# Performance work log

Hardware: AMD Instinct MI355X
Metric: run time of the kernel (lower is better)

## Reference

```python
import jax, jax.numpy as jnp
import numpy as np
import math

B, N, D, H = 4, 512, 256, 8
DH = D // H


def setup_inputs() -> dict:
    key = jax.random.key(0)
    ks = jax.random.split(key, 10)
    s = 1.0 / math.sqrt(D)
    return {
        "h": jax.random.normal(ks[0], (B, N, D), jnp.float32),
        "p": jax.random.uniform(ks[1], (B, N, 2), jnp.float32) * 100.0,
        "side_id": jax.random.randint(ks[2], (B, N), 0, 2),
        "mask": jnp.ones((B, N), dtype=bool),
        # weights stored in 'apply' orientation: y = x @ W (+ b)
        "Wq": jax.random.normal(ks[3], (D, D), jnp.float32) * s,
        "Wk": jax.random.normal(ks[4], (D, D), jnp.float32) * s,
        "Wv": jax.random.normal(ks[5], (D, D), jnp.float32) * s,
        "Wo": jax.random.normal(ks[6], (D, D), jnp.float32) * s,
        "W1": jax.random.normal(ks[7], (4, D), jnp.float32) * 0.5,
        "b1": jnp.zeros((D,), jnp.float32),
        "W2": jax.random.normal(ks[8], (D, H), jnp.float32) * s,
        "b2": jnp.zeros((H,), jnp.float32),
    }


def reference(h, p, side_id, mask, Wq, Wk, Wv, Wo, W1, b1, W2, b2):
    # zero out masked players
    h = jnp.where(mask[..., None], h, 0.0)  # [B,N,D]

    q = (h @ Wq).reshape(B, N, H, DH)
    k = (h @ Wk).reshape(B, N, H, DH)
    v = (h @ Wv).reshape(B, N, H, DH)

    # pairwise relative-position features [B,N,N,4]
    dp = p[:, :, None, :] - p[:, None, :, :]               # [B,N,N,2]
    dist = jnp.clip(jnp.linalg.norm(dp, axis=-1, keepdims=True), 1e-6)
    is_team = (side_id[:, :, None] == side_id[:, None, :]).astype(h.dtype)[..., None]
    feat = jnp.concatenate([dp, dist, is_team], axis=-1)

    # 2-layer bias MLP -> per-head bias [B,H,N,N]
    hid = jax.nn.relu(feat @ W1 + b1)                      # [B,N,N,D]
    bias = (hid @ W2 + b2).transpose(0, 3, 1, 2)           # [B,H,N,N]

    logits = jnp.einsum('bihd,bjhd->bhij', q, k) / math.sqrt(DH)
    logits = logits + bias
    logits = logits + jnp.where(mask, 0.0, -1e9)[:, None, None, :]  # key mask

    attn = jax.nn.softmax(logits, axis=-1)                 # dropout = identity (eval)
    out = jnp.einsum('bhij,bjhd->bihd', attn, v).reshape(B, N, D)
    return out @ Wo
```

## Files before the change

### kernel.cpp

```cpp
#include <hip/hip_runtime.h>
#include <math.h>

#define BB 4
#define NN 512
#define DD 256
#define HH 8
#define BND (BB*NN*DD)

typedef _Float16 h2 __attribute__((ext_vector_type(2)));
typedef _Float16 f16x4 __attribute__((ext_vector_type(4)));
typedef float    f32x4 __attribute__((ext_vector_type(4)));

static __device__ __forceinline__ h2 u2h(unsigned u) { return __builtin_bit_cast(h2, u); }
static __device__ __forceinline__ h2 pk2(float a, float b) {
    h2 r; r[0] = (_Float16)a; r[1] = (_Float16)b; return r;
}
static __device__ __forceinline__ unsigned pk2u(float a, float b) {
    return __builtin_bit_cast(unsigned, pk2(a, b));
}
static __device__ __forceinline__ h2 pkz(float a, float b) {
    return __builtin_bit_cast(h2, __builtin_amdgcn_cvt_pkrtz(a, b));
}
static __device__ __forceinline__ float dot2(h2 a, h2 b, float c) {
    return __builtin_amdgcn_fdot2(a, b, c, false);
}

__global__ __launch_bounds__(256) void pack_wt(
    const float* __restrict__ Wq, const float* __restrict__ Wk,
    const float* __restrict__ Wv, const float* __restrict__ Wo,
    _Float16* __restrict__ wt)
{
    __shared__ float T[64][65];
    const int t  = threadIdx.x;
    const int nb = blockIdx.x >> 2;
    const int kb = blockIdx.x & 3;
    const int tn = t & 63;
    const int tr = t >> 6;
    const int nbase = nb * 64;
    const float* W = (nbase < 256) ? Wq : (nbase < 512) ? Wk : (nbase < 768) ? Wv : Wo;
    const int noff = nbase & 255;
    #pragma unroll
    for (int r = 0; r < 16; ++r) {
        const int kl = tr*16 + r;
        T[kl][tn] = W[(size_t)(kb*64 + kl)*DD + noff + tn];
    }
    __syncthreads();
    #pragma unroll
    for (int r = 0; r < 16; ++r) {
        const int nl = tr*16 + r;
        wt[(size_t)(nbase + nl)*DD + kb*64 + tn] = (_Float16)T[tn][nl];
    }
}

__global__ __launch_bounds__(64) void gemm_qkv(
    const float* __restrict__ hg, const int* __restrict__ mask,
    const _Float16* __restrict__ wt,
    _Float16* __restrict__ q16, _Float16* __restrict__ k16, _Float16* __restrict__ v16h)
{
    const int l  = threadIdx.x;
    const int lo = l & 15, g = l >> 4;
    const int bid = blockIdx.x;
    const int rt = bid / 24, ct = bid % 24;
    const int R0 = rt*16, C0 = ct*32;
    const int row = R0 + lo;
    const float msc = (mask[row] != 0) ? 1.f : 0.f;

    const float*    xrow = hg + (size_t)row*DD;
    const _Float16* w0   = wt + (size_t)(C0 + lo)*DD;
    const _Float16* w1   = wt + (size_t)(C0 + 16 + lo)*DD;
    f32x4 ac0 = {0.f,0.f,0.f,0.f}, ac1 = {0.f,0.f,0.f,0.f};
    #pragma unroll
    for (int kk = 0; kk < 16; ++kk) {
        const float4 xv = *(const float4*)(xrow + kk*16 + g*4);
        f16x4 a;
        a[0] = (_Float16)(xv.x * msc);
        a[1] = (_Float16)(xv.y * msc);
        a[2] = (_Float16)(xv.z * msc);
        a[3] = (_Float16)(xv.w * msc);
        const f16x4 b0 = *(const f16x4*)(w0 + kk*16 + g*4);
        const f16x4 b1 = *(const f16x4*)(w1 + kk*16 + g*4);
        ac0 = __builtin_amdgcn_mfma_f32_16x16x16f16(a, b0, ac0, 0, 0, 0);
        ac1 = __builtin_amdgcn_mfma_f32_16x16x16f16(a, b1, ac1, 0, 0, 0);
    }
    const float qscale = 0.17677669529663687f;
    #pragma unroll
    for (int ci = 0; ci < 2; ++ci) {
        const f32x4 ac = ci ? ac1 : ac0;
        const int col = C0 + ci*16 + lo;
        const int seg = col >> 8;
        const int cc  = col & 255;
        #pragma unroll
        for (int r = 0; r < 4; ++r) {
            const int ro = R0 + g*4 + r;
            const float val = ac[r];
            if (seg == 0)      q16[(size_t)ro*DD + cc] = (_Float16)val;
            else if (seg == 1) k16[(size_t)ro*DD + cc] = (_Float16)(val * qscale);
            else               v16h[((size_t)(ro >> 1)*DD + cc)*2 + (ro & 1)] = (_Float16)val;
        }
    }
}

__global__ __launch_bounds__(256, 3) void bias_qk(
    const _Float16* __restrict__ q16, const _Float16* __restrict__ k16,
    const float* __restrict__ p, const int* __restrict__ side, const int* __restrict__ mask,
    const float* __restrict__ W1, const float* __restrict__ b1,
    const float* __restrict__ W2, const float* __restrict__ b2,
    unsigned* __restrict__ logitsH)
{
    __shared__ float bsm[4][16*132];
    __shared__ float pis[16][2];
    __shared__ int   sis[16];

    const int t  = threadIdx.x;
    const int w  = t >> 6;
    const int l  = t & 63;
    const int lo = l & 15;
    const int g  = l >> 4;

    const int bid = blockIdx.x;
    const int b   = bid >> 8;
    const int it  = (bid >> 3) & 31;
    const int je  = bid & 7;
    const int i0  = it * 16;
    const int jb  = je * 64 + w * 16;
    const int j   = jb + lo;

    if (t < 16) {
        const float2 pp = ((const float2*)p)[b*NN + i0 + t];
        pis[t][0] = pp.x; pis[t][1] = pp.y;
        sis[t] = side[b*NN + i0 + t];
    }
    __syncthreads();

    const f16x4 z4 = {(_Float16)0.f,(_Float16)0.f,(_Float16)0.f,(_Float16)0.f};
    const f32x4 zf = {0.f,0.f,0.f,0.f};
    const h2 zz = {(_Float16)0.f, (_Float16)0.f};

    f16x4 a1[16];
    #pragma unroll
    for (int m = 0; m < 16; ++m) {
        const int hid = m*16 + lo;
        f16x4 v = z4;
        const float w0 = W1[hid], w1 = W1[256+hid], w2 = W1[512+hid], w3 = W1[768+hid];
        const float bb1 = b1[hid];
        if (g == 0) { v[0]=(_Float16)w0; v[1]=(_Float16)w1; v[2]=(_Float16)w2; v[3]=(_Float16)w3; }
        else if (g == 1) { v[0]=(_Float16)bb1; }
        a1[m] = v;
    }
    f16x4 a2[16];
    #pragma unroll
    for (int s = 0; s < 16; ++s) {
        const int kb4 = s*16 + g*4;
        const int hs  = lo & 7;
        f16x4 v;
        v[0] = (_Float16)W2[(kb4+0)*HH + hs];
        v[1] = (_Float16)W2[(kb4+1)*HH + hs];
        v[2] = (_Float16)W2[(kb4+2)*HH + hs];
        v[3] = (_Float16)W2[(kb4+3)*HH + hs];
        a2[s] = (lo < 8) ? v : z4;
    }
    float b2v[4];
    #pragma unroll
    for (int r = 0; r < 4; ++r) b2v[r] = (g < 2) ? b2[(g*4 + r) & 7] : 0.f;

    const float2 pj = ((const float2*)p)[b*NN + j];
    const int   sj  = side[b*NN + j];
    const float km  = mask[b*NN + j] ? 0.f : -3.0e4f;

    float* bw = &bsm[w][0];

    #pragma unroll 2
    for (int i = 0; i < 16; ++i) {
        const float pix = pis[i][0], piy = pis[i][1];
        const int   sii = sis[i];
        const float dx = pix - pj.x;
        const float dy = piy - pj.y;
        const float di = fmaxf(sqrtf(dx*dx + dy*dy), 1e-6f);
        const float tm = (sii == sj) ? 1.f : 0.f;
        const h2 fA = pk2(dx, dy);
        const h2 fB = pk2(di, tm);
        f16x4 bf = z4;
        if (g == 0) { bf[0]=fA[0]; bf[1]=fA[1]; bf[2]=fB[0]; bf[3]=fB[1]; }
        else if (g == 1) { bf[0] = (_Float16)1.f; }

        f32x4 e0 = zf, e1 = zf;
        #pragma unroll
        for (int s = 0; s < 16; ++s) {
            const f32x4 c1 = __builtin_amdgcn_mfma_f32_16x16x16f16(a1[s], bf, zf, 0, 0, 0);
            const h2 p01 = pkz(c1[0], c1[1]);
            const h2 p23 = pkz(c1[2], c1[3]);
            const h2 r01 = __builtin_elementwise_max(p01, zz);
            const h2 r23 = __builtin_elementwise_max(p23, zz);
            f16x4 hb;
            hb[0]=r01[0]; hb[1]=r01[1]; hb[2]=r23[0]; hb[3]=r23[1];
            if (s & 1) e1 = __builtin_amdgcn_mfma_f32_16x16x16f16(a2[s], hb, e1, 0, 0, 0);
            else       e0 = __builtin_amdgcn_mfma_f32_16x16x16f16(a2[s], hb, e0, 0, 0, 0);
        }
        if (l < 32) {
            #pragma unroll
            for (int r = 0; r < 4; ++r)
                bw[i*132 + (g*4 + r)*16 + lo] = e0[r] + e1[r] + b2v[r] + km;
        }
    }

    asm volatile("s_waitcnt lgkmcnt(0)" ::: "memory");
    __builtin_amdgcn_sched_barrier(0);

    {
        const _Float16* qbase = q16 + (size_t)(b*NN + i0 + lo)*DD;
        const _Float16* kbase = k16 + (size_t)(b*NN + j)*DD;
        #pragma unroll
        for (int h = 0; h < 8; ++h) {
            const f16x4 q0  = *(const f16x4*)(qbase + h*32 + g*4);
            const f16x4 q1  = *(const f16x4*)(qbase + h*32 + 16 + g*4);
            const f16x4 kf0 = *(const f16x4*)(kbase + h*32 + g*4);
            const f16x4 kf1 = *(const f16x4*)(kbase + h*32 + 16 + g*4);
            f32x4 a  = __builtin_amdgcn_mfma_f32_16x16x16f16(q0, kf0, zf, 0, 0, 0);
            f32x4 qk = __builtin_amdgcn_mfma_f32_16x16x16f16(q1, kf1, a, 0, 0, 0);
            #pragma unroll
            for (int r = 0; r < 4; ++r)
                bw[(g*4 + r)*132 + h*16 + lo] += qk[r];
        }
    }

    asm volatile("s_waitcnt lgkmcnt(0)" ::: "memory");
    __builtin_amdgcn_sched_barrier(0);

    {
        const int hh = (l >> 3) & 7;
        const int jp = l & 7;
        #pragma unroll
        for (int u = 0; u < 16; ++u) {
            const float2 v2 = *(const float2*)&bw[u*132 + hh*16 + 2*jp];
            logitsH[((size_t)((b*NN + i0 + u)*HH + hh))*(NN/2) + (jb >> 1) + jp] =
                pk2u(v2.x, v2.y);
        }
    }
}

__global__ __launch_bounds__(256, 4) void attn_sm(
    const unsigned* __restrict__ logitsH, const unsigned* __restrict__ v16p,
    float* __restrict__ ao)
{
    __shared__ unsigned Lgh[16][260];
    __shared__ float red[16][16];
    __shared__ float mx[16];
    __shared__ float rs[16];

    const int t  = threadIdx.x;
    const int b  = blockIdx.x / (NN/2);
    const int i0 = (blockIdx.x % (NN/2)) * 2;

    #pragma unroll
    for (int ii = 0; ii < 2; ++ii)
        #pragma unroll
        for (int hh = 0; hh < HH; ++hh)
            Lgh[ii*8 + hh][t] = logitsH[((size_t)((b*NN + i0 + ii)*HH + hh))*(NN/2) + t];
    __syncthreads();

    const int combo = t >> 4;
    const int sub   = t & 15;
    {
        h2 pm = u2h(0xFC00FC00u);
        for (int jp = sub; jp < NN/2; jp += 16)
            pm = __builtin_elementwise_max(pm, u2h(Lgh[combo][jp]));
        red[combo][sub] = fmaxf((float)pm[0], (float)pm[1]);
    }
    __syncthreads();
    if (t < 16) {
        float mm = red[t][0];
        #pragma unroll
        for (int s = 1; s < 16; ++s) mm = fmaxf(mm, red[t][s]);
        mx[t] = mm;
    }
    __syncthreads();
    {
        const float M = mx[combo];
        float s = 0.f;
        for (int jp = sub; jp < NN/2; jp += 16) {
            const h2 lg = u2h(Lgh[combo][jp]);
            const float e0 = __expf((float)lg[0] - M);
            const float e1 = __expf((float)lg[1] - M);
            s += e0 + e1;
            Lgh[combo][jp] = pk2u(e0, e1);
        }
        red[combo][sub] = s;
    }
    __syncthreads();
    if (t < 16) {
        float s = 0.f;
        #pragma unroll
        for (int ss = 0; ss < 16; ++ss) s += red[t][ss];
        rs[t] = 1.f / s;
    }
    __syncthreads();

    {
        const int c = t;
        const int hh = c >> 5;
        const unsigned* vb = v16p + (size_t)b*(NN/2)*DD + c;
        float o[2] = {0.f, 0.f};
        for (int jp = 0; jp < NN/2; ++jp) {
            const h2 vp = u2h(vb[(size_t)jp*DD]);
            #pragma unroll
            for (int ii = 0; ii < 2; ++ii)
                o[ii] = dot2(u2h(Lgh[ii*8 + hh][jp]), vp, o[ii]);
        }
        #pragma unroll
        for (int ii = 0; ii < 2; ++ii)
            ao[(size_t)(b*NN + i0 + ii)*DD + c] = o[ii] * rs[ii*8 + hh];
    }
}

__global__ __launch_bounds__(64) void gemm_o(
    const float* __restrict__ X, const _Float16* __restrict__ wt,
    float* __restrict__ Y)
{
    const int l  = threadIdx.x;
    const int lo = l & 15, g = l >> 4;
    const int bid = blockIdx.x;
    const int rt = bid >> 3, ct = bid & 7;
    const int R0 = rt*16, C0 = ct*32;
    const int row = R0 + lo;

    const float*    xrow = X + (size_t)row*DD;
    const _Float16* w0   = wt + (size_t)(C0 + lo)*DD;
    const _Float16* w1   = wt + (size_t)(C0 + 16 + lo)*DD;
    f32x4 ac0 = {0.f,0.f,0.f,0.f}, ac1 = {0.f,0.f,0.f,0.f};
    #pragma unroll
    for (int kk = 0; kk < 16; ++kk) {
        const float4 xv = *(const float4*)(xrow + kk*16 + g*4);
        f16x4 a;
        a[0] = (_Float16)xv.x;
        a[1] = (_Float16)xv.y;
        a[2] = (_Float16)xv.z;
        a[3] = (_Float16)xv.w;
        const f16x4 b0 = *(const f16x4*)(w0 + kk*16 + g*4);
        const f16x4 b1 = *(const f16x4*)(w1 + kk*16 + g*4);
        ac0 = __builtin_amdgcn_mfma_f32_16x16x16f16(a, b0, ac0, 0, 0, 0);
        ac1 = __builtin_amdgcn_mfma_f32_16x16x16f16(a, b1, ac1, 0, 0, 0);
    }
    #pragma unroll
    for (int ci = 0; ci < 2; ++ci) {
        const f32x4 ac = ci ? ac1 : ac0;
        const int col = C0 + ci*16 + lo;
        #pragma unroll
        for (int r = 0; r < 4; ++r)
            Y[(size_t)(R0 + g*4 + r)*DD + col] = ac[r];
    }
}

extern "C" void kernel_launch(void* const* d_in, const int* in_sizes, int n_in,
                              void* d_out, int out_size, void* d_ws, size_t ws_size,
                              hipStream_t stream) {
    const float* hg   = (const float*)d_in[0];
    const float* p    = (const float*)d_in[1];
    const int*   side = (const int*)d_in[2];
    const int*   mask = (const int*)d_in[3];
    const float* Wq   = (const float*)d_in[4];
    const float* Wk   = (const float*)d_in[5];
    const float* Wv   = (const float*)d_in[6];
    const float* Wo   = (const float*)d_in[7];
    const float* W1   = (const float*)d_in[8];
    const float* b1   = (const float*)d_in[9];
    const float* W2   = (const float*)d_in[10];
    const float* b2   = (const float*)d_in[11];

    float* ws = (float*)d_ws;
    float* ao = ws;
    _Float16* q16 = (_Float16*)(ws + BND);
    _Float16* k16 = q16 + BND;
    _Float16* v16 = k16 + BND;
    unsigned* logitsH = (unsigned*)(v16 + BND);
    _Float16* wt16 = (_Float16*)(logitsH + (size_t)BB*NN*HH*(NN/2));

    pack_wt<<<64, 256, 0, stream>>>(Wq, Wk, Wv, Wo, wt16);
    gemm_qkv<<<128*24, 64, 0, stream>>>(hg, mask, wt16, q16, k16, v16);
    bias_qk<<<1024, 256, 0, stream>>>(q16, k16, p, side, mask, W1, b1, W2, b2, logitsH);
    attn_sm<<<BB*(NN/2), 256, 0, stream>>>(logitsH, (const unsigned*)v16, ao);
    gemm_o<<<128*8, 64, 0, stream>>>(ao, wt16 + (size_t)768*DD, (float*)d_out);
}
```

Baseline: 91.48 us.

## Fuse output projection into attention kernel and halve bias_qk row tile

The output projection (gemm_o) is folded into attn_sm. Each block keeps its two attention-output rows in LDS as fp16 and multiplies them by Wo^T with dot2 instructions, which removes a kernel launch and the fp32 ao round trip through global memory. Separately, bias_qk now processes 8 query rows per block instead of 16, doubling the grid and raising the launch-bounds occupancy hint from 3 to 8. The QK MFMA still computes 16 rows, so half of that work is wasted, and the fused Wo product reads the full weight matrix once per block with scalar-style dot products instead of MFMA.

```diff
diff --git a/kernel.cpp b/kernel.cpp
--- a/kernel.cpp
+++ b/kernel.cpp
@@ -100,16 +100,16 @@
     }
 }
 
-__global__ __launch_bounds__(256, 3) void bias_qk(
+__global__ __launch_bounds__(256, 8) void bias_qk(
     const _Float16* __restrict__ q16, const _Float16* __restrict__ k16,
     const float* __restrict__ p, const int* __restrict__ side, const int* __restrict__ mask,
     const float* __restrict__ W1, const float* __restrict__ b1,
     const float* __restrict__ W2, const float* __restrict__ b2,
     unsigned* __restrict__ logitsH)
 {
-    __shared__ float bsm[4][16*132];
-    __shared__ float pis[16][2];
-    __shared__ int   sis[16];
+    __shared__ float bsm[4][8*132];
+    __shared__ float pis[8][2];
+    __shared__ int   sis[8];
 
     const int t  = threadIdx.x;
     const int w  = t >> 6;
@@ -118,14 +118,14 @@
     const int g  = l >> 4;
 
     const int bid = blockIdx.x;
-    const int b   = bid >> 8;
-    const int it  = (bid >> 3) & 31;
+    const int b   = bid >> 9;
+    const int it  = (bid >> 3) & 63;
     const int je  = bid & 7;
-    const int i0  = it * 16;
+    const int i0  = it * 8;
     const int jb  = je * 64 + w * 16;
     const int j   = jb + lo;
 
-    if (t < 16) {
+    if (t < 8) {
         const float2 pp = ((const float2*)p)[b*NN + i0 + t];
         pis[t][0] = pp.x; pis[t][1] = pp.y;
         sis[t] = side[b*NN + i0 + t];
@@ -170,7 +170,7 @@
     float* bw = &bsm[w][0];
 
     #pragma unroll 2
-    for (int i = 0; i < 16; ++i) {
+    for (int i = 0; i < 8; ++i) {
         const float pix = pis[i][0], piy = pis[i][1];
         const int   sii = sis[i];
         const float dx = pix - pj.x;
@@ -207,7 +207,7 @@
     __builtin_amdgcn_sched_barrier(0);
 
     {
-        const _Float16* qbase = q16 + (size_t)(b*NN + i0 + lo)*DD;
+        const _Float16* qbase = q16 + (size_t)(b*NN + i0 + (lo & 7))*DD;
         const _Float16* kbase = k16 + (size_t)(b*NN + j)*DD;
         #pragma unroll
         for (int h = 0; h < 8; ++h) {
@@ -217,9 +217,11 @@
             const f16x4 kf1 = *(const f16x4*)(kbase + h*32 + 16 + g*4);
             f32x4 a  = __builtin_amdgcn_mfma_f32_16x16x16f16(q0, kf0, zf, 0, 0, 0);
             f32x4 qk = __builtin_amdgcn_mfma_f32_16x16x16f16(q1, kf1, a, 0, 0, 0);
-            #pragma unroll
-            for (int r = 0; r < 4; ++r)
-                bw[(g*4 + r)*132 + h*16 + lo] += qk[r];
+            if (g < 2) {
+                #pragma unroll
+                for (int r = 0; r < 4; ++r)
+                    bw[(g*4 + r)*132 + h*16 + lo] += qk[r];
+            }
         }
     }
 
@@ -230,7 +232,7 @@
         const int hh = (l >> 3) & 7;
         const int jp = l & 7;
         #pragma unroll
-        for (int u = 0; u < 16; ++u) {
+        for (int u = 0; u < 8; ++u) {
             const float2 v2 = *(const float2*)&bw[u*132 + hh*16 + 2*jp];
             logitsH[((size_t)((b*NN + i0 + u)*HH + hh))*(NN/2) + (jb >> 1) + jp] =
                 pk2u(v2.x, v2.y);
@@ -240,12 +242,14 @@
 
 __global__ __launch_bounds__(256, 4) void attn_sm(
     const unsigned* __restrict__ logitsH, const unsigned* __restrict__ v16p,
-    float* __restrict__ ao)
+    const _Float16* __restrict__ wo_t,
+    float* __restrict__ Y)
 {
     __shared__ unsigned Lgh[16][260];
     __shared__ float red[16][16];
     __shared__ float mx[16];
     __shared__ float rs[16];
+    __shared__ _Float16 aoL[2][DD];
 
     const int t  = threadIdx.x;
     const int b  = blockIdx.x / (NN/2);
@@ -308,45 +312,26 @@
         }
         #pragma unroll
         for (int ii = 0; ii < 2; ++ii)
-            ao[(size_t)(b*NN + i0 + ii)*DD + c] = o[ii] * rs[ii*8 + hh];
-    }
-}
-
-__global__ __launch_bounds__(64) void gemm_o(
-    const float* __restrict__ X, const _Float16* __restrict__ wt,
-    float* __restrict__ Y)
-{
-    const int l  = threadIdx.x;
-    const int lo = l & 15, g = l >> 4;
-    const int bid = blockIdx.x;
-    const int rt = bid >> 3, ct = bid & 7;
-    const int R0 = rt*16, C0 = ct*32;
-    const int row = R0 + lo;
-
-    const float*    xrow = X + (size_t)row*DD;
-    const _Float16* w0   = wt + (size_t)(C0 + lo)*DD;
-    const _Float16* w1   = wt + (size_t)(C0 + 16 + lo)*DD;
-    f32x4 ac0 = {0.f,0.f,0.f,0.f}, ac1 = {0.f,0.f,0.f,0.f};
-    #pragma unroll
-    for (int kk = 0; kk < 16; ++kk) {
-        const float4 xv = *(const float4*)(xrow + kk*16 + g*4);
-        f16x4 a;
-        a[0] = (_Float16)xv.x;
-        a[1] = (_Float16)xv.y;
-        a[2] = (_Float16)xv.z;
-        a[3] = (_Float16)xv.w;
-        const f16x4 b0 = *(const f16x4*)(w0 + kk*16 + g*4);
-        const f16x4 b1 = *(const f16x4*)(w1 + kk*16 + g*4);
-        ac0 = __builtin_amdgcn_mfma_f32_16x16x16f16(a, b0, ac0, 0, 0, 0);
-        ac1 = __builtin_amdgcn_mfma_f32_16x16x16f16(a, b1, ac1, 0, 0, 0);
-    }
-    #pragma unroll
-    for (int ci = 0; ci < 2; ++ci) {
-        const f32x4 ac = ci ? ac1 : ac0;
-        const int col = C0 + ci*16 + lo;
-        #pragma unroll
-        for (int r = 0; r < 4; ++r)
-            Y[(size_t)(R0 + g*4 + r)*DD + col] = ac[r];
+            aoL[ii][c] = (_Float16)(o[ii] * rs[ii*8 + hh]);
+    }
+    __syncthreads();
+
+    {
+        const f16x4* wrow = (const f16x4*)(wo_t + (size_t)t*DD);
+        float acc0 = 0.f, acc1 = 0.f;
+        #pragma unroll 8
+        for (int d4 = 0; d4 < DD/4; ++d4) {
+            const f16x4 wv = wrow[d4];
+            const f16x4 a0 = *(const f16x4*)&aoL[0][d4*4];
+            const f16x4 a1v = *(const f16x4*)&aoL[1][d4*4];
+            const h2 wlo = {wv[0], wv[1]}, whi = {wv[2], wv[3]};
+            acc0 = dot2(h2{a0[0], a0[1]},  wlo, acc0);
+            acc0 = dot2(h2{a0[2], a0[3]},  whi, acc0);
+            acc1 = dot2(h2{a1v[0], a1v[1]}, wlo, acc1);
+            acc1 = dot2(h2{a1v[2], a1v[3]}, whi, acc1);
+        }
+        Y[(size_t)(b*NN + i0)*DD + t]     = acc0;
+        Y[(size_t)(b*NN + i0 + 1)*DD + t] = acc1;
     }
 }
 
@@ -367,8 +352,7 @@
     const float* b2   = (const float*)d_in[11];
 
     float* ws = (float*)d_ws;
-    float* ao = ws;
-    _Float16* q16 = (_Float16*)(ws + BND);
+    _Float16* q16 = (_Float16*)(ws);
     _Float16* k16 = q16 + BND;
     _Float16* v16 = k16 + BND;
     unsigned* logitsH = (unsigned*)(v16 + BND);
@@ -376,7 +360,7 @@
 
     pack_wt<<<64, 256, 0, stream>>>(Wq, Wk, Wv, Wo, wt16);
     gemm_qkv<<<128*24, 64, 0, stream>>>(hg, mask, wt16, q16, k16, v16);
-    bias_qk<<<1024, 256, 0, stream>>>(q16, k16, p, side, mask, W1, b1, W2, b2, logitsH);
-    attn_sm<<<BB*(NN/2), 256, 0, stream>>>(logitsH, (const unsigned*)v16, ao);
-    gemm_o<<<128*8, 64, 0, stream>>>(ao, wt16 + (size_t)768*DD, (float*)d_out);
-}
+    bias_qk<<<2048, 256, 0, stream>>>(q16, k16, p, side, mask, W1, b1, W2, b2, logitsH);
+    attn_sm<<<BB*(NN/2), 256, 0, stream>>>(logitsH, (const unsigned*)v16,
+                                           wt16 + (size_t)768*DD, (float*)d_out);
+}
```

Measured after the change: 177.5 us. 1.94x slower.
